# Performance work log

Hardware: AMD Instinct MI355X
Metric: run time of the kernel (lower is better)

Reference implementation:

```python
import jax, jax.numpy as jnp
import numpy as np
import math

B, NOUT, NCLASSES, CENTER, TOPK = 1024, 512, 5994, 3, 5
M, SUB_M, SCALE = 0.2, -0.06, 30.0

COS_M, SIN_M = math.cos(M), math.sin(M)
TH, MM = math.cos(math.pi - M), math.sin(math.pi - M) * M
SUB_COS_M, SUB_SIN_M = math.cos(SUB_M), math.sin(SUB_M)
SUB_TH, SUB_MM = math.cos(math.pi - SUB_M), math.sin(math.pi - SUB_M) * SUB_M


def setup_inputs() -> dict:
    key = jax.random.key(0)
    k1, k2, k3 = jax.random.split(key, 3)
    x = jax.random.normal(k1, (B, NOUT), dtype=jnp.float32)
    # xavier_normal over (center, nClasses, nOut): fan_in=nClasses*nOut, fan_out=center*nOut
    std = math.sqrt(2.0 / (NCLASSES * NOUT + CENTER * NOUT))
    weight = jax.random.normal(k2, (CENTER, NCLASSES, NOUT), dtype=jnp.float32) * std
    label = jax.random.randint(k3, (B,), 0, NCLASSES, dtype=jnp.int64)
    return {"x": x, "weight": weight, "label": label}


def _l2norm(v, axis=-1, eps=1e-12):
    return v / jnp.maximum(jnp.linalg.norm(v, axis=axis, keepdims=True), eps)


def reference(x, weight, label):
    xn = _l2norm(x)                       # [B, j]
    wn = _l2norm(weight)                  # [a, c, j]
    cosine_subcen = jnp.einsum('bj,acj->bac', xn, wn)   # [B, center, C]
    cosine = jnp.max(cosine_subcen, axis=1)             # [B, C]

    sine = jnp.sqrt(jnp.clip(1.0 - cosine * cosine, 0.0, 1.0))
    phi = jnp.where(cosine - TH > 0, cosine * COS_M - sine * SIN_M, cosine - MM)
    sub_phi = jnp.where(cosine - SUB_TH > 0,
                        cosine * SUB_COS_M - sine * SUB_SIN_M,
                        cosine - SUB_MM)

    # topk+1 candidates; drop the label column if present, else drop the last
    _, idx = jax.lax.top_k(cosine, TOPK + 1)            # [B, topk+1]
    is_label = (idx == label[:, None].astype(idx.dtype))
    # stable sort pushes the (unique) label hit to the end, preserving order otherwise
    order = jnp.argsort(is_label.astype(jnp.int32), axis=1, stable=True)
    idx_fixed = jnp.take_along_axis(idx, order[:, :TOPK], axis=1)   # [B, topk]

    rows = jnp.arange(B)[:, None]
    one_hot_sub = jnp.zeros_like(cosine).at[rows, idx_fixed].add(1.0)
    one_hot = jax.nn.one_hot(label, NCLASSES, dtype=cosine.dtype)

    output = (one_hot * phi + one_hot_sub * sub_phi
              + (1.0 - one_hot_sub - one_hot) * cosine) * SCALE

    logp = jax.nn.log_softmax(output, axis=-1)
    loss = -jnp.mean(logp[jnp.arange(B), label])

    pred = jnp.argmax(cosine * SCALE, axis=-1)
    prec1 = jnp.mean((pred == label).astype(jnp.float32)) * 100.0
    return loss, prec1
```

## Files before the change

kernel.cpp:

```cpp
#include <hip/hip_runtime.h>
#include <math.h>

#define NB 1024
#define NC 5994
#define NCP 6144
#define NCS 6016
#define NK 512
#define NA 3
#define NT 48
#define SCALE_F 30.0f

#define COS_M_F 0.9800665778412416f
#define SIN_M_F 0.19866933079506122f
#define TH_F (-0.9800665778412416f)
#define MM_F 0.039733866159012244f
#define SUB_COS_M_F 0.9982005399352042f
#define SUB_SIN_M_F (-0.05996400647944459f)
#define SUB_TH_F (-0.9982005399352042f)
#define SUB_MM_F 0.0035978403887666754f

typedef __attribute__((ext_vector_type(8))) short short8;
typedef __attribute__((ext_vector_type(8))) unsigned short ushort8;
typedef __attribute__((ext_vector_type(4))) float f32x4;

__device__ __forceinline__ float waveReduceSum(float v) {
#pragma unroll
  for (int off = 32; off > 0; off >>= 1) v += __shfl_down(v, off);
  return v;
}

__device__ __forceinline__ void waveArgMax(float& v, int& i) {
#pragma unroll
  for (int off = 32; off > 0; off >>= 1) {
    float ov = __shfl_down(v, off);
    int oi = __shfl_down(i, off);
    if (ov > v || (ov == v && (unsigned)oi < (unsigned)i)) { v = ov; i = oi; }
  }
}

__device__ __forceinline__ ushort f2bf(float f) {
  unsigned u = __float_as_uint(f);
  u += 0x7FFFu + ((u >> 16) & 1u);
  return (ushort)(u >> 16);
}

__device__ __forceinline__ float bf2f(ushort u) {
  return __uint_as_float(((unsigned)u) << 16);
}

__device__ __forceinline__ void load_lds16(const ushort* g, ushort* l) {
  __builtin_amdgcn_global_load_lds(
      (const __attribute__((address_space(1))) unsigned int*)g,
      (__attribute__((address_space(3))) unsigned int*)l, 16, 0, 0);
}

__global__ __launch_bounds__(256) void norm_convert(const float* __restrict__ x,
                                                    const float* __restrict__ w,
                                                    ushort* __restrict__ xb,
                                                    ushort* __restrict__ wb) {
  const int row = blockIdx.x * 4 + (threadIdx.x >> 6);
  const int lane = threadIdx.x & 63;
  const float* src;
  ushort* dst;
  if (row < NB) {
    src = x + (size_t)row * NK;
    dst = xb + (size_t)row * NK;
  } else {
    const int r = row - NB;
    const int a = r / NCP, c = r % NCP;
    dst = wb + (size_t)r * NK;
    if (c >= NC) {
      ushort4 z = {0, 0, 0, 0};
      *(ushort4*)(dst + lane * 4) = z;
      *(ushort4*)(dst + 256 + lane * 4) = z;
      return;
    }
    src = w + ((size_t)a * NC + c) * NK;
  }
  const float4 v0 = *(const float4*)(src + lane * 4);
  const float4 v1 = *(const float4*)(src + 256 + lane * 4);
  float ss = v0.x * v0.x + v0.y * v0.y + v0.z * v0.z + v0.w * v0.w +
             v1.x * v1.x + v1.y * v1.y + v1.z * v1.z + v1.w * v1.w;
  ss = waveReduceSum(ss);
  ss = __shfl(ss, 0);
  const float rn = 1.0f / fmaxf(sqrtf(ss), 1e-12f);
  ushort4 o0 = {f2bf(v0.x * rn), f2bf(v0.y * rn), f2bf(v0.z * rn), f2bf(v0.w * rn)};
  ushort4 o1 = {f2bf(v1.x * rn), f2bf(v1.y * rn), f2bf(v1.z * rn), f2bf(v1.w * rn)};
  *(ushort4*)(dst + lane * 4) = o0;
  *(ushort4*)(dst + 256 + lane * 4) = o1;
}

__global__ __launch_bounds__(128) void cos_gemm_mfma(const ushort* __restrict__ Xb,
                                                     const ushort* __restrict__ Wb,
                                                     ushort* __restrict__ cosb) {
  __shared__ ushort sA0[64 * 32];
  __shared__ ushort sA1[64 * 32];
  __shared__ ushort sB0[128 * 32];
  __shared__ ushort sB1[128 * 32];
  const int tid = threadIdx.x;
  const int lane = tid & 63;
  const int w = tid >> 6;

  const int id = blockIdx.x;
  const int cx = (id & 7) + ((id >> 7) << 3);
  const int by = (id >> 3) & 15;
  const int b0 = by * 64;
  const int c0 = cx * 128;

  const int lrow = lane >> 2;
  const int skg = ((lane & 3) - ((lane >> 3) & 3)) & 3;
  const ushort* gA = Xb + (size_t)(b0 + w * 32 + lrow) * NK + skg * 8;
  const ushort* gB = Wb + (size_t)(c0 + w * 64 + lrow) * NK + skg * 8;
  const int ldsA = w * 1024;
  const int ldsB = w * 2048;
  const int w4 = w * 4;

  const int r = lane & 15;
  const int kg = lane >> 4;
  const int rdoff = r * 32 + (((kg + (r >> 1)) & 3) * 8);

  f32x4 best[4][4];
  f32x4 acc[4][4];
#pragma unroll
  for (int i = 0; i < 4; ++i)
#pragma unroll
    for (int j = 0; j < 4; ++j) {
#pragma unroll
      for (int q = 0; q < 4; ++q) best[i][j][q] = -INFINITY;
      acc[i][j] = (f32x4)(0.f);
    }

  load_lds16(gA, (ushort*)sA0 + ldsA);
  load_lds16(gA + 16 * NK, (ushort*)sA0 + ldsA + 512);
#pragma unroll
  for (int j = 0; j < 4; ++j)
    load_lds16(gB + (size_t)j * 16 * NK, (ushort*)sB0 + ldsB + j * 512);
  __syncthreads();

#define GEMM_BODY(T, SAr, SBr, SAw, SBw)                                        \
  {                                                                             \
    const int t_ = (T);                                                         \
    if (t_ + 1 < NT) {                                                          \
      const int tn = t_ + 1;                                                    \
      const int k0 = (tn & 15) << 5;                                            \
      const size_t boff = (size_t)(tn >> 4) * NCP * NK + k0;                    \
      load_lds16(gA + k0, (ushort*)SAw + ldsA);                                 \
      load_lds16(gA + k0 + 16 * NK, (ushort*)SAw + ldsA + 512);                 \
      _Pragma("unroll") for (int j = 0; j < 4; ++j)                             \
          load_lds16(gB + boff + (size_t)j * 16 * NK,                           \
                     (ushort*)SBw + ldsB + j * 512);                            \
    }                                                                           \
    short8 af[4], bf[4];                                                        \
    _Pragma("unroll") for (int mi = 0; mi < 4; ++mi)                            \
        af[mi] = *(const short8*)&SAr[mi * 512 + rdoff];                        \
    _Pragma("unroll") for (int ni = 0; ni < 4; ++ni)                            \
        bf[ni] = *(const short8*)&SBr[(w4 + ni) * 512 + rdoff];                 \
    _Pragma("unroll") for (int mi = 0; mi < 4; ++mi)                            \
        _Pragma("unroll") for (int ni = 0; ni < 4; ++ni)                        \
            acc[mi][ni] = __builtin_amdgcn_mfma_f32_16x16x32_bf16(              \
                af[mi], bf[ni], acc[mi][ni], 0, 0, 0);                          \
    if ((t_ & 15) == 15) {                                                      \
      _Pragma("unroll") for (int i = 0; i < 4; ++i)                             \
          _Pragma("unroll") for (int j = 0; j < 4; ++j) {                       \
        _Pragma("unroll") for (int q = 0; q < 4; ++q)                           \
            best[i][j][q] = fmaxf(best[i][j][q], acc[i][j][q]);                 \
        acc[i][j] = (f32x4)(0.f);                                               \
      }                                                                         \
    }                                                                           \
    __syncthreads();                                                            \
  }

  for (int t = 0; t < NT; t += 2) {
    GEMM_BODY(t, sA0, sB0, sA1, sB1)
    GEMM_BODY(t + 1, sA1, sB1, sA0, sB0)
  }
#undef GEMM_BODY

  const int q4 = (lane >> 4) * 4;
#pragma unroll
  for (int ni = 0; ni < 4; ++ni) {
    const int col = c0 + w * 64 + ni * 16 + r;
    if (col < NC) {
#pragma unroll
      for (int mi = 0; mi < 4; ++mi) {
        const int row0 = b0 + mi * 16 + q4;
#pragma unroll
        for (int q = 0; q < 4; ++q)
          cosb[(size_t)(row0 + q) * NCS + col] = f2bf(best[mi][ni][q]);
      }
    }
  }
}

__global__ __launch_bounds__(256) void row_loss(const ushort* __restrict__ cosb,
                                                const int* __restrict__ label,
                                                float* __restrict__ loss_b,
                                                float* __restrict__ corr_b) {
  __shared__ float swv[4];
  __shared__ int swi[4];
  __shared__ float s_red[4];
  __shared__ float s_maxv;
  __shared__ float s_cosL;
  __shared__ float topv[6];
  __shared__ int topi[6];

  const int b = blockIdx.x, tid = threadIdx.x;
  const int wv = tid >> 6;
  const int lab = label[b];
  const ushort* row = cosb + (size_t)b * NCS;

  float v[24];
  float bv = -INFINITY;
  int bi = -1;
#pragma unroll
  for (int j = 0; j < 3; ++j) {
    const ushort8 u = *(const ushort8*)(row + j * 2048 + tid * 8);
#pragma unroll
    for (int e = 0; e < 8; ++e) {
      const int idx = j * 2048 + tid * 8 + e;
      const float f = (idx < NC) ? bf2f(u[e]) : -INFINITY;
      v[j * 8 + e] = f;
      if (f > bv) { bv = f; bi = idx; }
      if (idx == lab) s_cosL = f;
    }
  }
  waveArgMax(bv, bi);
  if ((tid & 63) == 0) { swv[wv] = bv; swi[wv] = bi; }
  __syncthreads();
  if (tid == 0) {
    float mv = swv[0]; int mi = swi[0];
    for (int q = 1; q < 4; ++q)
      if (swv[q] > mv || (swv[q] == mv && (unsigned)swi[q] < (unsigned)mi)) { mv = swv[q]; mi = swi[q]; }
    s_maxv = mv; topv[0] = mv; topi[0] = mi;
  }
  __syncthreads();
  const float maxv = s_maxv;

  float ps = 0.f;
#pragma unroll
  for (int j = 0; j < 24; ++j) ps += __expf(SCALE_F * (v[j] - maxv));
  ps = waveReduceSum(ps);
  if ((tid & 63) == 0) s_red[wv] = ps;

  unsigned excl = 0;
  {
    const int wi = topi[0];
    if (((wi & 2047) >> 3) == tid) excl |= 1u << (((wi >> 11) << 3) | (wi & 7));
  }

  for (int e = 1; e < 6; ++e) {
    float lv = -INFINITY;
    int li = -1;
#pragma unroll
    for (int j = 0; j < 3; ++j)
#pragma unroll
      for (int k = 0; k < 8; ++k) {
        const int s = j * 8 + k;
        if (!((excl >> s) & 1u) && v[s] > lv) { lv = v[s]; li = j * 2048 + tid * 8 + k; }
      }
    waveArgMax(lv, li);
    if ((tid & 63) == 0) { swv[wv] = lv; swi[wv] = li; }
    __syncthreads();
    if (tid == 0) {
      float mv = swv[0]; int mi = swi[0];
      for (int q = 1; q < 4; ++q)
        if (swv[q] > mv || (swv[q] == mv && (unsigned)swi[q] < (unsigned)mi)) { mv = swv[q]; mi = swi[q]; }
      topv[e] = mv; topi[e] = mi;
    }
    __syncthreads();
    const int wi = topi[e];
    if (((wi & 2047) >> 3) == tid) excl |= 1u << (((wi >> 11) << 3) | (wi & 7));
  }

  if (tid == 0) {
    const float S = s_red[0] + s_red[1] + s_red[2] + s_red[3];
    const float m = SCALE_F * maxv;
    const float cosL = s_cosL;
    const float sineL = sqrtf(fminf(fmaxf(1.f - cosL * cosL, 0.f), 1.f));
    const float phiL = (cosL - TH_F > 0.f) ? (cosL * COS_M_F - sineL * SIN_M_F) : (cosL - MM_F);
    float adj = __expf(SCALE_F * phiL - m) - __expf(SCALE_F * cosL - m);
    int cnt = 0;
    for (int e = 0; e < 6 && cnt < 5; ++e) {
      if (topi[e] == lab) continue;
      const float c = topv[e];
      const float sine = sqrtf(fminf(fmaxf(1.f - c * c, 0.f), 1.f));
      const float sp = (c - SUB_TH_F > 0.f) ? (c * SUB_COS_M_F - sine * SUB_SIN_M_F) : (c - SUB_MM_F);
      adj += __expf(SCALE_F * sp - m) - __expf(SCALE_F * c - m);
      ++cnt;
    }
    const float Sp = S + adj;
    loss_b[b] = (logf(Sp) + m) - SCALE_F * phiL;
    corr_b[b] = (topi[0] == lab) ? 1.f : 0.f;
  }
}

__global__ __launch_bounds__(256) void finalize(const float* __restrict__ loss_b,
                                                const float* __restrict__ corr_b,
                                                float* __restrict__ out) {
  const int tid = threadIdx.x;
  float ls = 0.f, cs = 0.f;
  for (int i = tid; i < NB; i += 256) { ls += loss_b[i]; cs += corr_b[i]; }
  ls = waveReduceSum(ls);
  cs = waveReduceSum(cs);
  __shared__ float sl[4], sc[4];
  if ((tid & 63) == 0) { sl[tid >> 6] = ls; sc[tid >> 6] = cs; }
  __syncthreads();
  if (tid == 0) {
    const float L = sl[0] + sl[1] + sl[2] + sl[3];
    const float Cr = sc[0] + sc[1] + sc[2] + sc[3];
    out[0] = L / (float)NB;
    out[1] = Cr / (float)NB * 100.f;
  }
}

extern "C" void kernel_launch(void* const* d_in, const int* in_sizes, int n_in,
                              void* d_out, int out_size, void* d_ws, size_t ws_size,
                              hipStream_t stream) {
  const float* x = (const float*)d_in[0];
  const float* w = (const float*)d_in[1];
  const int* label = (const int*)d_in[2];
  float* out = (float*)d_out;
  char* ws = (char*)d_ws;

  ushort* xb = (ushort*)ws;
  ushort* wb = (ushort*)(ws + 1048576);
  ushort* cosb = (ushort*)(ws + 1048576 + 18874368);
  float* loss_b = (float*)ws;
  float* corr_b = (float*)(ws + 4096);

  norm_convert<<<(NB + NA * NCP) / 4, 256, 0, stream>>>(x, w, xb, wb);
  cos_gemm_mfma<<<16 * 48, 128, 0, stream>>>(xb, wb, cosb);
  row_loss<<<NB, 256, 0, stream>>>(cosb, label, loss_b, corr_b);
  finalize<<<1, 256, 0, stream>>>(loss_b, corr_b, out);
}
```

Before: 65.60 us.

## Replicate normalized X per XCD and remap conversion blocks to match GEMM XCD placement

The normalize/convert kernel now writes eight copies of the bf16 X matrix, one per XCD. Its block-to-row mapping is changed so that the W rows each XCD will later read are produced on that same XCD. The GEMM reads its A tile from the copy for its own XCD, so data written by the previous kernel is meant to stay in the local L2 instead of crossing dies. The cost is more blocks and 8x the X write traffic, plus a larger workspace.

```diff
diff --git a/kernel.cpp b/kernel.cpp
--- a/kernel.cpp
+++ b/kernel.cpp
@@ -56,19 +56,26 @@
 
 __global__ __launch_bounds__(256) void norm_convert(const float* __restrict__ x,
                                                     const float* __restrict__ w,
-                                                    ushort* __restrict__ xb,
+                                                    ushort* __restrict__ xbR,
                                                     ushort* __restrict__ wb) {
-  const int row = blockIdx.x * 4 + (threadIdx.x >> 6);
+  const int id = blockIdx.x;
+  const int xcd = id & 7;
+  const int j = id >> 3;
+  const int wv = threadIdx.x >> 6;
   const int lane = threadIdx.x & 63;
   const float* src;
   ushort* dst;
-  if (row < NB) {
+  if (j >= 576) {
+    const int row = (j - 576) * 4 + wv;
     src = x + (size_t)row * NK;
-    dst = xb + (size_t)row * NK;
+    dst = xbR + ((size_t)xcd * NB + row) * NK;
   } else {
-    const int r = row - NB;
-    const int a = r / NCP, c = r % NCP;
-    dst = wb + (size_t)r * NK;
+    const int pc = j >> 5;
+    const int r4 = j & 31;
+    const int p = (pc / 3) * 8 + xcd;
+    const int a = pc % 3;
+    const int c = p * 128 + r4 * 4 + wv;
+    dst = wb + ((size_t)a * NCP + c) * NK;
     if (c >= NC) {
       ushort4 z = {0, 0, 0, 0};
       *(ushort4*)(dst + lane * 4) = z;
@@ -90,7 +97,7 @@
   *(ushort4*)(dst + 256 + lane * 4) = o1;
 }
 
-__global__ __launch_bounds__(128) void cos_gemm_mfma(const ushort* __restrict__ Xb,
+__global__ __launch_bounds__(128) void cos_gemm_mfma(const ushort* __restrict__ XbR,
                                                      const ushort* __restrict__ Wb,
                                                      ushort* __restrict__ cosb) {
   __shared__ ushort sA0[64 * 32];
@@ -102,14 +109,15 @@
   const int w = tid >> 6;
 
   const int id = blockIdx.x;
-  const int cx = (id & 7) + ((id >> 7) << 3);
+  const int resid = id & 7;
+  const int cx = resid + ((id >> 7) << 3);
   const int by = (id >> 3) & 15;
   const int b0 = by * 64;
   const int c0 = cx * 128;
 
   const int lrow = lane >> 2;
   const int skg = ((lane & 3) - ((lane >> 3) & 3)) & 3;
-  const ushort* gA = Xb + (size_t)(b0 + w * 32 + lrow) * NK + skg * 8;
+  const ushort* gA = XbR + ((size_t)resid * NB + b0 + w * 32 + lrow) * NK + skg * 8;
   const ushort* gB = Wb + (size_t)(c0 + w * 64 + lrow) * NK + skg * 8;
   const int ldsA = w * 1024;
   const int ldsB = w * 2048;
@@ -322,14 +330,14 @@
   float* out = (float*)d_out;
   char* ws = (char*)d_ws;
 
-  ushort* xb = (ushort*)ws;
-  ushort* wb = (ushort*)(ws + 1048576);
-  ushort* cosb = (ushort*)(ws + 1048576 + 18874368);
+  ushort* xbR = (ushort*)ws;
+  ushort* wb = (ushort*)(ws + 8388608);
+  ushort* cosb = (ushort*)(ws + 8388608 + 18874368);
   float* loss_b = (float*)ws;
   float* corr_b = (float*)(ws + 4096);
 
-  norm_convert<<<(NB + NA * NCP) / 4, 256, 0, stream>>>(x, w, xb, wb);
-  cos_gemm_mfma<<<16 * 48, 128, 0, stream>>>(xb, wb, cosb);
+  norm_convert<<<8 * 832, 256, 0, stream>>>(x, w, xbR, wb);
+  cos_gemm_mfma<<<16 * 48, 128, 0, stream>>>(xbR, wb, cosb);
   row_loss<<<NB, 256, 0, stream>>>(cosb, label, loss_b, corr_b);
   finalize<<<1, 256, 0, stream>>>(loss_b, corr_b, out);
 }
```

New measurement: 68.60 us. 4.6% more time.

## Split subcenter dimension across GEMM blocks and reduce max in row_loss

Applied to the files above, without the earlier changes.

The cosine GEMM grid is split three ways along the subcenter axis, so each block runs 16 k-steps instead of 48 and writes its own per-subcenter bf16 cosine plane. row_loss then reads all three planes and takes the elementwise max. This triples the block count to improve CU occupancy and latency hiding. In exchange it adds about three times the intermediate cosine write and read traffic and needs a larger workspace, falling back to the old path if the workspace is too small.

```diff
diff --git a/kernel.cpp b/kernel.cpp
--- a/kernel.cpp
+++ b/kernel.cpp
@@ -7,7 +7,6 @@
 #define NCS 6016
 #define NK 512
 #define NA 3
-#define NT 48
 #define SCALE_F 30.0f
 
 #define COS_M_F 0.9800665778412416f
@@ -90,6 +89,7 @@
   *(ushort4*)(dst + 256 + lane * 4) = o1;
 }
 
+template <int SPLIT>
 __global__ __launch_bounds__(128) void cos_gemm_mfma(const ushort* __restrict__ Xb,
                                                      const ushort* __restrict__ Wb,
                                                      ushort* __restrict__ cosb) {
@@ -100,17 +100,28 @@
   const int tid = threadIdx.x;
   const int lane = tid & 63;
   const int w = tid >> 6;
+  const int NTloc = SPLIT ? 16 : 48;
 
   const int id = blockIdx.x;
-  const int cx = (id & 7) + ((id >> 7) << 3);
-  const int by = (id >> 3) & 15;
+  int cx, by, a0;
+  if (SPLIT) {
+    const int t1 = id >> 3;
+    const int mid = t1 % 48;
+    cx = (id & 7) + (t1 / 48) * 8;
+    by = mid & 15;
+    a0 = mid >> 4;
+  } else {
+    cx = (id & 7) + ((id >> 7) << 3);
+    by = (id >> 3) & 15;
+    a0 = 0;
+  }
   const int b0 = by * 64;
   const int c0 = cx * 128;
 
   const int lrow = lane >> 2;
   const int skg = ((lane & 3) - ((lane >> 3) & 3)) & 3;
   const ushort* gA = Xb + (size_t)(b0 + w * 32 + lrow) * NK + skg * 8;
-  const ushort* gB = Wb + (size_t)(c0 + w * 64 + lrow) * NK + skg * 8;
+  const ushort* gB = Wb + ((size_t)a0 * NCP + c0 + w * 64 + lrow) * NK + skg * 8;
   const int ldsA = w * 1024;
   const int ldsB = w * 2048;
   const int w4 = w * 4;
@@ -140,7 +151,7 @@
 #define GEMM_BODY(T, SAr, SBr, SAw, SBw)                                        \
   {                                                                             \
     const int t_ = (T);                                                         \
-    if (t_ + 1 < NT) {                                                          \
+    if (t_ + 1 < NTloc) {                                                       \
       const int tn = t_ + 1;                                                    \
       const int k0 = (tn & 15) << 5;                                            \
       const size_t boff = (size_t)(tn >> 4) * NCP * NK + k0;                    \
@@ -170,12 +181,13 @@
     __syncthreads();                                                            \
   }
 
-  for (int t = 0; t < NT; t += 2) {
+  for (int t = 0; t < NTloc; t += 2) {
     GEMM_BODY(t, sA0, sB0, sA1, sB1)
     GEMM_BODY(t + 1, sA1, sB1, sA0, sB0)
   }
 #undef GEMM_BODY
 
+  ushort* dstbase = cosb + (SPLIT ? (size_t)a0 * NB * NCS : 0);
   const int q4 = (lane >> 4) * 4;
 #pragma unroll
   for (int ni = 0; ni < 4; ++ni) {
@@ -186,12 +198,13 @@
         const int row0 = b0 + mi * 16 + q4;
 #pragma unroll
         for (int q = 0; q < 4; ++q)
-          cosb[(size_t)(row0 + q) * NCS + col] = f2bf(best[mi][ni][q]);
+          dstbase[(size_t)(row0 + q) * NCS + col] = f2bf(best[mi][ni][q]);
       }
     }
   }
 }
 
+template <int SPLIT>
 __global__ __launch_bounds__(256) void row_loss(const ushort* __restrict__ cosb,
                                                 const int* __restrict__ label,
                                                 float* __restrict__ loss_b,
@@ -207,18 +220,29 @@
   const int b = blockIdx.x, tid = threadIdx.x;
   const int wv = tid >> 6;
   const int lab = label[b];
-  const ushort* row = cosb + (size_t)b * NCS;
+  const ushort* row0 = cosb + (size_t)b * NCS;
+  const ushort* row1 = row0 + (size_t)NB * NCS;
+  const ushort* row2 = row1 + (size_t)NB * NCS;
 
   float v[24];
   float bv = -INFINITY;
   int bi = -1;
 #pragma unroll
   for (int j = 0; j < 3; ++j) {
-    const ushort8 u = *(const ushort8*)(row + j * 2048 + tid * 8);
+    const int off = j * 2048 + tid * 8;
+    const ushort8 u0 = *(const ushort8*)(row0 + off);
+    ushort8 u1, u2;
+    if (SPLIT) { u1 = *(const ushort8*)(row1 + off); u2 = *(const ushort8*)(row2 + off); }
 #pragma unroll
     for (int e = 0; e < 8; ++e) {
-      const int idx = j * 2048 + tid * 8 + e;
-      const float f = (idx < NC) ? bf2f(u[e]) : -INFINITY;
+      const int idx = off + e;
+      float f;
+      if (SPLIT) {
+        f = fmaxf(fmaxf(bf2f(u0[e]), bf2f(u1[e])), bf2f(u2[e]));
+      } else {
+        f = bf2f(u0[e]);
+      }
+      f = (idx < NC) ? f : -INFINITY;
       v[j * 8 + e] = f;
       if (f > bv) { bv = f; bi = idx; }
       if (idx == lab) s_cosL = f;
@@ -328,8 +352,16 @@
   float* loss_b = (float*)ws;
   float* corr_b = (float*)(ws + 4096);
 
+  const size_t needed_split = 1048576u + 18874368u + 3u * (size_t)NB * NCS * 2u + 8192u;
+  const bool use_split = (ws_size >= needed_split);
+
   norm_convert<<<(NB + NA * NCP) / 4, 256, 0, stream>>>(x, w, xb, wb);
-  cos_gemm_mfma<<<16 * 48, 128, 0, stream>>>(xb, wb, cosb);
-  row_loss<<<NB, 256, 0, stream>>>(cosb, label, loss_b, corr_b);
+  if (use_split) {
+    cos_gemm_mfma<1><<<2304, 128, 0, stream>>>(xb, wb, cosb);
+    row_loss<1><<<NB, 256, 0, stream>>>(cosb, label, loss_b, corr_b);
+  } else {
+    cos_gemm_mfma<0><<<16 * 48, 128, 0, stream>>>(xb, wb, cosb);
+    row_loss<0><<<NB, 256, 0, stream>>>(cosb, label, loss_b, corr_b);
+  }
   finalize<<<1, 256, 0, stream>>>(loss_b, corr_b, out);
 }
```

Measured after the change: 69.36 us. 5.7% more time.
